# Performance work log

Measured on AMD Instinct MI355X. Metric: run time of the kernel, lower is better.

Reference implementation:

```python
import jax, jax.numpy as jnp
import numpy as np

B, IN, H = 8192, 1024, 1024

def _ln(x, g, b, eps=1e-5):
    mu = jnp.mean(x, axis=-1, keepdims=True)
    var = jnp.mean(jnp.square(x - mu), axis=-1, keepdims=True)
    return (x - mu) * jax.lax.rsqrt(var + eps) * g + b

def setup_inputs() -> dict:
    key = jax.random.key(0)
    ks = jax.random.split(key, 8)
    s_h = 1.0 / np.sqrt(H)
    s_i = 1.0 / np.sqrt(IN)
    inp = {
        'x': jax.random.normal(ks[0], (B, IN), jnp.float32),
        'h': jax.random.normal(ks[1], (B, H), jnp.float32),
        'W_r': jax.random.uniform(ks[2], (H, H), jnp.float32, -s_h, s_h),
        'U_r': jax.random.uniform(ks[3], (H, IN), jnp.float32, -s_i, s_i),
        'W_u': jax.random.uniform(ks[4], (H, H), jnp.float32, -s_h, s_h),
        'U_u': jax.random.uniform(ks[5], (H, IN), jnp.float32, -s_i, s_i),
        'W_c': jax.random.uniform(ks[6], (H, H), jnp.float32, -s_h, s_h),
        'U_c': jax.random.uniform(ks[7], (H, IN), jnp.float32, -s_i, s_i),
        # LayerNorm params: rows = [r_hidden, r_input, u_hidden, u_input, c_hidden, c_input]
        'ln_gamma': 0.1 * jnp.ones((6, H), jnp.float32),
        'ln_beta': jnp.zeros((6, H), jnp.float32),
    }
    return inp

def reference(x, h, W_r, U_r, W_u, U_u, W_c, U_c, ln_gamma, ln_beta):
    g, b = ln_gamma, ln_beta
    # nn.Linear(bias=False): y = x @ W.T
    r = jax.nn.sigmoid(_ln(h @ W_r.T, g[0], b[0]) + _ln(x @ U_r.T, g[1], b[1]))
    u = jax.nn.sigmoid(_ln(h @ W_u.T, g[2], b[2]) + _ln(x @ U_u.T, g[3], b[3]))
    c = jnp.tanh(_ln((h * r) @ W_c.T, g[4], b[4]) + _ln(x @ U_c.T, g[5], b[5]))
    return (1.0 - u) * h + u * c
```

## Files before the change

### kernel.cpp

```cpp
#include <hip/hip_runtime.h>
#include <cstdint>
#include <cstddef>

typedef unsigned short u16;
typedef unsigned char u8;
typedef __attribute__((ext_vector_type(4))) float f32x4;
typedef __attribute__((ext_vector_type(4))) int i32x4;
typedef __attribute__((ext_vector_type(8))) int i32x8;

__device__ inline float bf2f(u16 u) { return __uint_as_float(((unsigned)u) << 16); }
__device__ inline unsigned f2bf(float f) {
  unsigned u = __float_as_uint(f);
  u += 0x7fffu + ((u >> 16) & 1u);
  return u >> 16;
}

__device__ inline unsigned f2fp8(float f) {
  unsigned s = (__float_as_uint(f) >> 31) << 7;
  float a = fabsf(f);
  if (a >= 0.015625f) {
    unsigned u = __float_as_uint(a);
    u += 0x7FFFFu + ((u >> 20) & 1u);
    unsigned e = (u >> 23) - 120u;
    unsigned m = (u >> 20) & 7u;
    return s | (e << 3) | m;
  }
  int m = (int)rintf(a * 512.0f);
  return s | (unsigned)m;
}

__device__ inline void async16(const void* g, void* l) {
  __builtin_amdgcn_global_load_lds(
      (const __attribute__((address_space(1))) void*)g,
      (__attribute__((address_space(3))) void*)l, 16, 0, 0);
}

__device__ inline i32x8 join8(i32x4 lo, i32x4 hi) {
  i32x8 r;
  r[0] = lo[0]; r[1] = lo[1]; r[2] = lo[2]; r[3] = lo[3];
  r[4] = hi[0]; r[5] = hi[1]; r[6] = hi[2]; r[7] = hi[3];
  return r;
}

__device__ inline void unpack8(uint4 q, float* o) {
  o[0] = bf2f((u16)(q.x & 0xffffu)); o[1] = bf2f((u16)(q.x >> 16));
  o[2] = bf2f((u16)(q.y & 0xffffu)); o[3] = bf2f((u16)(q.y >> 16));
  o[4] = bf2f((u16)(q.z & 0xffffu)); o[5] = bf2f((u16)(q.z >> 16));
  o[6] = bf2f((u16)(q.w & 0xffffu)); o[7] = bf2f((u16)(q.w >> 16));
}

__device__ inline float fast_sigmoid(float z) {
  return 1.0f / (1.0f + exp2f(-1.4426950408889634f * z));
}
__device__ inline float fast_tanh(float z) {
  return 1.0f - 2.0f / (1.0f + exp2f(2.8853900817779268f * z));
}

#define SB0() __builtin_amdgcn_sched_barrier(0)

struct ConvArgs3 {
  const float* x; const float* h;
  const float* w[6];
  u8* x8; u8* h8;
  u8* w8[6];
};

__global__ __launch_bounds__(256) void convert_all(ConvArgs3 a) {
  const int b = blockIdx.x;
  const int t = threadIdx.x;
  if (b < 16384) {
    const bool isx = b < 8192;
    const int off = isx ? b : b - 8192;
    const float* __restrict__ s = isx ? a.x : a.h;
    u8* __restrict__ d8 = isx ? a.x8 : a.h8;
    const int i = (off * 256 + t) * 4;
    float4 v = *(const float4*)(s + i);
    unsigned q = f2fp8(v.x) | (f2fp8(v.y) << 8) | (f2fp8(v.z) << 16) | (f2fp8(v.w) << 24);
    *(unsigned*)(d8 + i) = q;
  } else {
    const int tt = b - 16384;
    const int which = tt >> 10;
    const int off = tt & 1023;
    const float* __restrict__ s = a.w[which];
    u8* __restrict__ d8 = a.w8[which];
    const int i = (off * 256 + t) * 4;
    float4 v = *(const float4*)(s + i);
    unsigned q = f2fp8(v.x * 8192.f) | (f2fp8(v.y * 8192.f) << 8) |
                 (f2fp8(v.z * 8192.f) << 16) | (f2fp8(v.w * 8192.f) << 24);
    *(unsigned*)(d8 + i) = q;
  }
}

struct GemmF8 { const u8* A[4]; const u8* Bw[4]; u16* Y[4]; };

template <int NG>
__global__ __launch_bounds__(512, 2) void gemm_fp8(GemmF8 args) {
  const int p = blockIdx.x;
  const int wg = (p & 7) * (NG * 16) + (p >> 3);
  const int gate = wg >> 7;
  const int rem  = wg & 127;
  const int rblk = rem >> 2;
  const int cblk = rem & 3;

  const u8* __restrict__ A  = args.A[gate];
  const u8* __restrict__ Bw = args.Bw[gate];
  u16* __restrict__ Y = args.Y[gate];

  __shared__ __attribute__((aligned(16))) u8 sm[2][2][2][128 * 128];

  const int tid  = threadIdx.x;
  const int lane = tid & 63;
  const int w    = tid >> 6;
  const int wm   = w >> 2;
  const int wn   = w & 3;

  const int l8   = lane >> 3;
  const int sgrp = (lane & 7) ^ l8;
  const u8* aSrc = A  + ((size_t)(rblk * 256 + w * 8 + l8) << 10) + sgrp * 16;
  const u8* bSrc = Bw + ((size_t)(cblk * 256 + w * 8 + l8) << 10) + sgrp * 16;
  const int ldsW = w * 8 * 128;

  const int sw = lane & 7;
  const int g0 = (lane >> 4) * 2;
  const int o0 = ((g0 ^ sw) << 4);
  const int o1 = (((g0 + 1) ^ sw) << 4);
  const int frR = (lane & 15) * 128;

  f32x4 acc_lo[4][4] = {};
  f32x4 acc_hi[4][4] = {};

  auto stage = [&](const u8* src, int tt, int op, int half) {
    const int d = tt & 1;
    const u8* s = src + (size_t)half * 131072 + tt * 128;
    u8* l0 = &sm[d][op][half][ldsW];
    async16(s, l0);
    async16(s + 65536, l0 + 8192);
  };

  stage(bSrc, 0, 1, 0); stage(bSrc, 0, 1, 1);
  stage(aSrc, 0, 0, 0); stage(aSrc, 0, 0, 1);
  stage(bSrc, 1, 1, 0); stage(bSrc, 1, 1, 1);
  stage(aSrc, 1, 0, 0);
  asm volatile("s_waitcnt vmcnt(6)" ::: "memory");
  __builtin_amdgcn_s_barrier();

  i32x8 alo[4], bfg[4], ahi[4];
  {
    const u8* baseA = &sm[0][0][wm][0];
    const u8* baseB = &sm[0][1][wn >> 1][(wn & 1) * 8192];
#pragma unroll
    for (int m = 0; m < 4; ++m) {
      const int ra = frR + m * 2048;
      alo[m] = join8(*(const i32x4*)&baseA[ra + o0], *(const i32x4*)&baseA[ra + o1]);
    }
#pragma unroll
    for (int n = 0; n < 4; ++n) {
      const int rbb = frR + n * 2048;
      bfg[n] = join8(*(const i32x4*)&baseB[rbb + o0], *(const i32x4*)&baseB[rbb + o1]);
    }
  }
  SB0();

  for (int t = 0; t < 8; ++t) {
    const int d = t & 1;
    const u8* baseA  = &sm[d][0][wm][0];
    const u8* baseA2 = &sm[d ^ 1][0][wm][0];
    const u8* baseB2 = &sm[d ^ 1][1][wn >> 1][(wn & 1) * 8192];

    if (t + 1 < 8) stage(aSrc, t + 1, 0, 1);
    SB0();
    __builtin_amdgcn_s_barrier();
    asm volatile("s_waitcnt lgkmcnt(4)" ::: "memory");
    SB0();
    __builtin_amdgcn_s_setprio(1);
#pragma unroll
    for (int m = 0; m < 4; ++m)
#pragma unroll
      for (int n = 0; n < 2; ++n)
        acc_lo[m][n] = __builtin_amdgcn_mfma_scale_f32_16x16x128_f8f6f4(
            alo[m], bfg[n], acc_lo[m][n], 0, 0, 0, 127, 0, 114);
    __builtin_amdgcn_s_setprio(0);
    SB0();
    __builtin_amdgcn_s_barrier();

    if (t + 2 < 8) stage(bSrc, t + 2, 1, 0);
    SB0();
    __builtin_amdgcn_s_barrier();
    asm volatile("s_waitcnt lgkmcnt(0)" ::: "memory");
    SB0();
    __builtin_amdgcn_s_setprio(1);
#pragma unroll
    for (int m = 0; m < 4; ++m)
#pragma unroll
      for (int n = 2; n < 4; ++n)
        acc_lo[m][n] = __builtin_amdgcn_mfma_scale_f32_16x16x128_f8f6f4(
            alo[m], bfg[n], acc_lo[m][n], 0, 0, 0, 127, 0, 114);
    __builtin_amdgcn_s_setprio(0);
    SB0();
#pragma unroll
    for (int m = 0; m < 4; ++m) {
      const int ra = frR + m * 2048 + 8192;
      ahi[m] = join8(*(const i32x4*)&baseA[ra + o0], *(const i32x4*)&baseA[ra + o1]);
    }
    SB0();
    __builtin_amdgcn_s_barrier();

    if (t + 2 < 8) stage(bSrc, t + 2, 1, 1);
    SB0();
    __builtin_amdgcn_s_barrier();
    asm volatile("s_waitcnt lgkmcnt(0)" ::: "memory");
    SB0();
    __builtin_amdgcn_s_setprio(1);
#pragma unroll
    for (int m = 0; m < 4; ++m)
#pragma unroll
      for (int n = 0; n < 2; ++n)
        acc_hi[m][n] = __builtin_amdgcn_mfma_scale_f32_16x16x128_f8f6f4(
            ahi[m], bfg[n], acc_hi[m][n], 0, 0, 0, 127, 0, 114);
    __builtin_amdgcn_s_setprio(0);
    SB0();
    __builtin_amdgcn_s_barrier();

    if (t + 2 < 8) stage(aSrc, t + 2, 0, 0);
    SB0();
    __builtin_amdgcn_s_barrier();
    __builtin_amdgcn_s_setprio(1);
#pragma unroll
    for (int m = 0; m < 4; ++m)
#pragma unroll
      for (int n = 2; n < 4; ++n)
        acc_hi[m][n] = __builtin_amdgcn_mfma_scale_f32_16x16x128_f8f6f4(
            ahi[m], bfg[n], acc_hi[m][n], 0, 0, 0, 127, 0, 114);
    __builtin_amdgcn_s_setprio(0);
    SB0();
    if (t < 6) asm volatile("s_waitcnt vmcnt(6)" ::: "memory");
    else       asm volatile("s_waitcnt vmcnt(0)" ::: "memory");
    SB0();
    if (t + 1 < 8) {
#pragma unroll
      for (int m = 0; m < 4; ++m) {
        const int ra = frR + m * 2048;
        alo[m] = join8(*(const i32x4*)&baseA2[ra + o0], *(const i32x4*)&baseA2[ra + o1]);
      }
#pragma unroll
      for (int n = 0; n < 4; ++n) {
        const int rbb = frR + n * 2048;
        bfg[n] = join8(*(const i32x4*)&baseB2[rbb + o0], *(const i32x4*)&baseB2[rbb + o1]);
      }
    }
    SB0();
    __builtin_amdgcn_s_barrier();
  }

  const int rBase = rblk * 256 + wm * 128 + (lane >> 4) * 4;
  const int cBase = cblk * 256 + wn * 64 + (lane & 15);
#pragma unroll
  for (int m = 0; m < 4; ++m) {
#pragma unroll
    for (int i = 0; i < 4; ++i) {
      const size_t r0 = (size_t)(rBase + m * 16 + i) * 1024 + cBase;
#pragma unroll
      for (int n = 0; n < 4; ++n) {
        Y[r0 + n * 16]             = (u16)f2bf(acc_lo[m][n][i]);
        Y[r0 + 64 * 1024 + n * 16] = (u16)f2bf(acc_hi[m][n][i]);
      }
    }
  }
}

__global__ __launch_bounds__(256) void rgate_kernel(
    const u16* __restrict__ Yrh, const u16* __restrict__ Yrx,
    const float* __restrict__ h, const float* __restrict__ gamma,
    const float* __restrict__ beta, u8* __restrict__ hr8) {
  const int row  = blockIdx.x * 4 + (threadIdx.x >> 6);
  const int lane = threadIdx.x & 63;
  const size_t rb = (size_t)row * 1024;

  uint4 qa[2], qb[2];
  float4 hf[4];
#pragma unroll
  for (int c = 0; c < 2; c++) {
    const int cb = c * 512 + lane * 8;
    qa[c] = *(const uint4*)(Yrh + rb + cb);
    qb[c] = *(const uint4*)(Yrx + rb + cb);
    hf[c * 2]     = *(const float4*)(h + rb + cb);
    hf[c * 2 + 1] = *(const float4*)(h + rb + cb + 4);
  }

  float s0 = 0.f, s0q = 0.f, s1 = 0.f, s1q = 0.f;
  float tmp[8];
#pragma unroll
  for (int c = 0; c < 2; c++) {
    unpack8(qa[c], tmp);
#pragma unroll
    for (int j = 0; j < 8; j++) { s0 += tmp[j]; s0q += tmp[j] * tmp[j]; }
    unpack8(qb[c], tmp);
#pragma unroll
    for (int j = 0; j < 8; j++) { s1 += tmp[j]; s1q += tmp[j] * tmp[j]; }
  }
#pragma unroll
  for (int off = 1; off < 64; off <<= 1) {
    s0 += __shfl_xor(s0, off, 64);  s0q += __shfl_xor(s0q, off, 64);
    s1 += __shfl_xor(s1, off, 64);  s1q += __shfl_xor(s1q, off, 64);
  }

  const float inv = 1.0f / 1024.0f;
  const float mu0 = s0 * inv, rs0 = rsqrtf(s0q * inv - mu0 * mu0 + 1e-5f);
  const float mu1 = s1 * inv, rs1 = rsqrtf(s1q * inv - mu1 * mu1 + 1e-5f);

#pragma unroll
  for (int c = 0; c < 2; c++) {
    const int cb = c * 512 + lane * 8;
    float va[8], vb[8], o[8];
    unpack8(qa[c], va); unpack8(qb[c], vb);
    const float* hv = (const float*)&hf[c * 2];
#pragma unroll
    for (int j = 0; j < 8; j++) {
      const float ln0 = (va[j] - mu0) * rs0 * gamma[cb + j] + beta[cb + j];
      const float ln1 = (vb[j] - mu1) * rs1 * gamma[1024 + cb + j] + beta[1024 + cb + j];
      const float rg = fast_sigmoid(ln0 + ln1);
      o[j] = hv[j] * rg;
    }
    uint2 q;
    q.x = f2fp8(o[0]) | (f2fp8(o[1]) << 8) | (f2fp8(o[2]) << 16) | (f2fp8(o[3]) << 24);
    q.y = f2fp8(o[4]) | (f2fp8(o[5]) << 8) | (f2fp8(o[6]) << 16) | (f2fp8(o[7]) << 24);
    *(uint2*)(hr8 + rb + cb) = q;
  }
}

__global__ __launch_bounds__(256) void final_fuse(
    const u16* __restrict__ Yuh, const u16* __restrict__ Yux,
    const u16* __restrict__ Ych, const u16* __restrict__ Ycx,
    const float* __restrict__ h, const float* __restrict__ gamma,
    const float* __restrict__ beta, float* __restrict__ out) {
  const int row  = blockIdx.x * 4 + (threadIdx.x >> 6);
  const int lane = threadIdx.x & 63;
  const size_t rb = (size_t)row * 1024;

  uint4 q0[2], q1[2], q2[2], q3[2];
  float4 hf[4];
#pragma unroll
  for (int c = 0; c < 2; c++) {
    const int cb = c * 512 + lane * 8;
    q0[c] = *(const uint4*)(Yuh + rb + cb);
    q1[c] = *(const uint4*)(Yux + rb + cb);
    q2[c] = *(const uint4*)(Ych + rb + cb);
    q3[c] = *(const uint4*)(Ycx + rb + cb);
    hf[c * 2]     = *(const float4*)(h + rb + cb);
    hf[c * 2 + 1] = *(const float4*)(h + rb + cb + 4);
  }

  float s[8] = {0.f, 0.f, 0.f, 0.f, 0.f, 0.f, 0.f, 0.f};
  float tmp[8];
#pragma unroll
  for (int c = 0; c < 2; c++) {
    unpack8(q0[c], tmp);
#pragma unroll
    for (int j = 0; j < 8; j++) { s[0] += tmp[j]; s[1] += tmp[j] * tmp[j]; }
    unpack8(q1[c], tmp);
#pragma unroll
    for (int j = 0; j < 8; j++) { s[2] += tmp[j]; s[3] += tmp[j] * tmp[j]; }
    unpack8(q2[c], tmp);
#pragma unroll
    for (int j = 0; j < 8; j++) { s[4] += tmp[j]; s[5] += tmp[j] * tmp[j]; }
    unpack8(q3[c], tmp);
#pragma unroll
    for (int j = 0; j < 8; j++) { s[6] += tmp[j]; s[7] += tmp[j] * tmp[j]; }
  }
#pragma unroll
  for (int off = 1; off < 64; off <<= 1) {
#pragma unroll
    for (int q = 0; q < 8; q++) s[q] += __shfl_xor(s[q], off, 64);
  }

  const float inv = 1.0f / 1024.0f;
  const float mu0 = s[0] * inv, rs0 = rsqrtf(s[1] * inv - mu0 * mu0 + 1e-5f);
  const float mu1 = s[2] * inv, rs1 = rsqrtf(s[3] * inv - mu1 * mu1 + 1e-5f);
  const float mu2 = s[4] * inv, rs2 = rsqrtf(s[5] * inv - mu2 * mu2 + 1e-5f);
  const float mu3 = s[6] * inv, rs3 = rsqrtf(s[7] * inv - mu3 * mu3 + 1e-5f);

#pragma unroll
  for (int c = 0; c < 2; c++) {
    const int cb = c * 512 + lane * 8;
    float v0[8], v1[8], v2[8], v3[8];
    unpack8(q0[c], v0); unpack8(q1[c], v1); unpack8(q2[c], v2); unpack8(q3[c], v3);
    const float* hv = (const float*)&hf[c * 2];
    float o[8];
#pragma unroll
    for (int j = 0; j < 8; j++) {
      const int cc = cb + j;
      const float ln2 = (v0[j] - mu0) * rs0 * gamma[2 * 1024 + cc] + beta[2 * 1024 + cc];
      const float ln3 = (v1[j] - mu1) * rs1 * gamma[3 * 1024 + cc] + beta[3 * 1024 + cc];
      const float ln4 = (v2[j] - mu2) * rs2 * gamma[4 * 1024 + cc] + beta[4 * 1024 + cc];
      const float ln5 = (v3[j] - mu3) * rs3 * gamma[5 * 1024 + cc] + beta[5 * 1024 + cc];
      const float u  = fast_sigmoid(ln2 + ln3);
      const float cg = fast_tanh(ln4 + ln5);
      o[j] = (1.0f - u) * hv[j] + u * cg;
    }
    *(float4*)(out + rb + cb)     = *(float4*)&o[0];
    *(float4*)(out + rb + cb + 4) = *(float4*)&o[4];
  }
}

extern "C" void kernel_launch(void* const* d_in, const int* in_sizes, int n_in,
                              void* d_out, int out_size, void* d_ws, size_t ws_size,
                              hipStream_t stream) {
  const float* x  = (const float*)d_in[0];
  const float* h  = (const float*)d_in[1];
  const float* W_r = (const float*)d_in[2];
  const float* U_r = (const float*)d_in[3];
  const float* W_u = (const float*)d_in[4];
  const float* U_u = (const float*)d_in[5];
  const float* W_c = (const float*)d_in[6];
  const float* U_c = (const float*)d_in[7];
  const float* gamma = (const float*)d_in[8];
  const float* beta  = (const float*)d_in[9];
  float* out = (float*)d_out;

  char* ws = (char*)d_ws;
  const size_t MB = 1024 * 1024;

  u8* x8  = (u8*)(ws);
  u8* h8  = (u8*)(ws + 8 * MB);
  u8* hr8 = (u8*)(ws + 16 * MB);
  u8* w8[6];
  for (int i = 0; i < 6; i++) w8[i] = (u8*)(ws + 24 * MB + i * MB);
  u16* Y0 = (u16*)(ws + 32 * MB);
  u16* Y1 = (u16*)(ws + 48 * MB);
  u16* Y2 = (u16*)(ws + 64 * MB);
  u16* Y3 = (u16*)(ws + 80 * MB);
  u16* Y5 = (u16*)(ws + 96 * MB);

  ConvArgs3 ca = {};
  ca.x = x; ca.h = h;
  ca.w[0] = W_r; ca.w[1] = U_r; ca.w[2] = W_u; ca.w[3] = U_u; ca.w[4] = W_c; ca.w[5] = U_c;
  ca.x8 = x8; ca.h8 = h8;
  for (int i = 0; i < 6; i++) ca.w8[i] = w8[i];
  convert_all<<<22528, 256, 0, stream>>>(ca);

  GemmF8 gA = {};
  gA.A[0] = h8; gA.Bw[0] = w8[0]; gA.Y[0] = Y0;
  gA.A[1] = x8; gA.Bw[1] = w8[1]; gA.Y[1] = Y1;
  gA.A[2] = x8; gA.Bw[2] = w8[3]; gA.Y[2] = Y3;
  gA.A[3] = x8; gA.Bw[3] = w8[5]; gA.Y[3] = Y5;
  gemm_fp8<4><<<512, 512, 0, stream>>>(gA);

  rgate_kernel<<<2048, 256, 0, stream>>>(Y0, Y1, h, gamma, beta, hr8);

  GemmF8 gB = {};
  gB.A[0] = h8;  gB.Bw[0] = w8[2]; gB.Y[0] = Y2;
  gB.A[1] = hr8; gB.Bw[1] = w8[4]; gB.Y[1] = Y0;
  gemm_fp8<2><<<256, 512, 0, stream>>>(gB);

  final_fuse<<<2048, 256, 0, stream>>>(Y2, Y3, Y0, Y5, h, gamma, beta, out);
}
```

Before: 241.3 us.

## Shrink FP8 GEMM tiles to 128x128 with 4 waves and simpler double buffering

```diff
diff --git a/kernel.cpp b/kernel.cpp
--- a/kernel.cpp
+++ b/kernel.cpp
@@ -94,176 +94,103 @@
 struct GemmF8 { const u8* A[4]; const u8* Bw[4]; u16* Y[4]; };
 
 template <int NG>
-__global__ __launch_bounds__(512, 2) void gemm_fp8(GemmF8 args) {
+__global__ __launch_bounds__(256, 2) void gemm_f8s(GemmF8 args) {
   const int p = blockIdx.x;
-  const int wg = (p & 7) * (NG * 16) + (p >> 3);
-  const int gate = wg >> 7;
-  const int rem  = wg & 127;
-  const int rblk = rem >> 2;
-  const int cblk = rem & 3;
+  const int wg = (p & 7) * (NG * 64) + (p >> 3);
+  const int gate = wg >> 9;
+  const int rem  = wg & 511;
+  const int rblk = rem >> 3;
+  const int cblk = rem & 7;
 
   const u8* __restrict__ A  = args.A[gate];
   const u8* __restrict__ Bw = args.Bw[gate];
   u16* __restrict__ Y = args.Y[gate];
 
-  __shared__ __attribute__((aligned(16))) u8 sm[2][2][2][128 * 128];
+  __shared__ __attribute__((aligned(16))) u8 smA[2][128 * 128];
+  __shared__ __attribute__((aligned(16))) u8 smB[2][128 * 128];
 
   const int tid  = threadIdx.x;
   const int lane = tid & 63;
   const int w    = tid >> 6;
-  const int wm   = w >> 2;
-  const int wn   = w & 3;
+  const int wm   = w >> 1;
+  const int wn   = w & 1;
 
   const int l8   = lane >> 3;
   const int sgrp = (lane & 7) ^ l8;
-  const u8* aSrc = A  + ((size_t)(rblk * 256 + w * 8 + l8) << 10) + sgrp * 16;
-  const u8* bSrc = Bw + ((size_t)(cblk * 256 + w * 8 + l8) << 10) + sgrp * 16;
-  const int ldsW = w * 8 * 128;
+  const u8* aSrc = A  + ((size_t)(rblk * 128 + w * 32 + l8) << 10) + sgrp * 16;
+  const u8* bSrc = Bw + ((size_t)(cblk * 128 + w * 32 + l8) << 10) + sgrp * 16;
 
   const int sw = lane & 7;
   const int g0 = (lane >> 4) * 2;
   const int o0 = ((g0 ^ sw) << 4);
   const int o1 = (((g0 + 1) ^ sw) << 4);
-  const int frR = (lane & 15) * 128;
-
-  f32x4 acc_lo[4][4] = {};
-  f32x4 acc_hi[4][4] = {};
-
-  auto stage = [&](const u8* src, int tt, int op, int half) {
-    const int d = tt & 1;
-    const u8* s = src + (size_t)half * 131072 + tt * 128;
-    u8* l0 = &sm[d][op][half][ldsW];
-    async16(s, l0);
-    async16(s + 65536, l0 + 8192);
+  const int frA = (wm * 64 + (lane & 15)) * 128;
+  const int frB = (wn * 64 + (lane & 15)) * 128;
+
+  f32x4 acc[4][4] = {};
+
+  auto stage = [&](int tt) {
+    const int cur = tt & 1;
+    const size_t ko = (size_t)tt * 128;
+#pragma unroll
+    for (int i = 0; i < 4; ++i) {
+      async16(aSrc + (size_t)i * 8192 + ko, &smA[cur][(w * 32 + i * 8) * 128]);
+      async16(bSrc + (size_t)i * 8192 + ko, &smB[cur][(w * 32 + i * 8) * 128]);
+    }
   };
 
-  stage(bSrc, 0, 1, 0); stage(bSrc, 0, 1, 1);
-  stage(aSrc, 0, 0, 0); stage(aSrc, 0, 0, 1);
-  stage(bSrc, 1, 1, 0); stage(bSrc, 1, 1, 1);
-  stage(aSrc, 1, 0, 0);
-  asm volatile("s_waitcnt vmcnt(6)" ::: "memory");
+  stage(0);
+  stage(1);
+  asm volatile("s_waitcnt vmcnt(8)" ::: "memory");
   __builtin_amdgcn_s_barrier();
 
-  i32x8 alo[4], bfg[4], ahi[4];
-  {
-    const u8* baseA = &sm[0][0][wm][0];
-    const u8* baseB = &sm[0][1][wn >> 1][(wn & 1) * 8192];
+  for (int t = 0; t < 8; ++t) {
+    const int cur = t & 1;
+    const u8* bA = &smA[cur][0];
+    const u8* bB = &smB[cur][0];
+
+    i32x8 af[4], bf[4];
 #pragma unroll
     for (int m = 0; m < 4; ++m) {
-      const int ra = frR + m * 2048;
-      alo[m] = join8(*(const i32x4*)&baseA[ra + o0], *(const i32x4*)&baseA[ra + o1]);
+      const int ra = frA + m * 2048;
+      af[m] = join8(*(const i32x4*)&bA[ra + o0], *(const i32x4*)&bA[ra + o1]);
     }
 #pragma unroll
     for (int n = 0; n < 4; ++n) {
-      const int rbb = frR + n * 2048;
-      bfg[n] = join8(*(const i32x4*)&baseB[rbb + o0], *(const i32x4*)&baseB[rbb + o1]);
-    }
-  }
-  SB0();
-
-  for (int t = 0; t < 8; ++t) {
-    const int d = t & 1;
-    const u8* baseA  = &sm[d][0][wm][0];
-    const u8* baseA2 = &sm[d ^ 1][0][wm][0];
-    const u8* baseB2 = &sm[d ^ 1][1][wn >> 1][(wn & 1) * 8192];
-
-    if (t + 1 < 8) stage(aSrc, t + 1, 0, 1);
+      const int rb = frB + n * 2048;
+      bf[n] = join8(*(const i32x4*)&bB[rb + o0], *(const i32x4*)&bB[rb + o1]);
+    }
+    asm volatile("s_waitcnt lgkmcnt(0)" ::: "memory");
     SB0();
     __builtin_amdgcn_s_barrier();
-    asm volatile("s_waitcnt lgkmcnt(4)" ::: "memory");
+
+    if (t + 2 < 8) stage(t + 2);
     SB0();
     __builtin_amdgcn_s_setprio(1);
 #pragma unroll
     for (int m = 0; m < 4; ++m)
 #pragma unroll
-      for (int n = 0; n < 2; ++n)
-        acc_lo[m][n] = __builtin_amdgcn_mfma_scale_f32_16x16x128_f8f6f4(
-            alo[m], bfg[n], acc_lo[m][n], 0, 0, 0, 127, 0, 114);
+      for (int n = 0; n < 4; ++n)
+        acc[m][n] = __builtin_amdgcn_mfma_scale_f32_16x16x128_f8f6f4(
+            af[m], bf[n], acc[m][n], 0, 0, 0, 127, 0, 114);
     __builtin_amdgcn_s_setprio(0);
     SB0();
-    __builtin_amdgcn_s_barrier();
-
-    if (t + 2 < 8) stage(bSrc, t + 2, 1, 0);
+    if (t < 6)      asm volatile("s_waitcnt vmcnt(8)" ::: "memory");
+    else if (t == 6) asm volatile("s_waitcnt vmcnt(0)" ::: "memory");
     SB0();
     __builtin_amdgcn_s_barrier();
-    asm volatile("s_waitcnt lgkmcnt(0)" ::: "memory");
-    SB0();
-    __builtin_amdgcn_s_setprio(1);
-#pragma unroll
-    for (int m = 0; m < 4; ++m)
-#pragma unroll
-      for (int n = 2; n < 4; ++n)
-        acc_lo[m][n] = __builtin_amdgcn_mfma_scale_f32_16x16x128_f8f6f4(
-            alo[m], bfg[n], acc_lo[m][n], 0, 0, 0, 127, 0, 114);
-    __builtin_amdgcn_s_setprio(0);
-    SB0();
-#pragma unroll
-    for (int m = 0; m < 4; ++m) {
-      const int ra = frR + m * 2048 + 8192;
-      ahi[m] = join8(*(const i32x4*)&baseA[ra + o0], *(const i32x4*)&baseA[ra + o1]);
-    }
-    SB0();
-    __builtin_amdgcn_s_barrier();
-
-    if (t + 2 < 8) stage(bSrc, t + 2, 1, 1);
-    SB0();
-    __builtin_amdgcn_s_barrier();
-    asm volatile("s_waitcnt lgkmcnt(0)" ::: "memory");
-    SB0();
-    __builtin_amdgcn_s_setprio(1);
-#pragma unroll
-    for (int m = 0; m < 4; ++m)
-#pragma unroll
-      for (int n = 0; n < 2; ++n)
-        acc_hi[m][n] = __builtin_amdgcn_mfma_scale_f32_16x16x128_f8f6f4(
-            ahi[m], bfg[n], acc_hi[m][n], 0, 0, 0, 127, 0, 114);
-    __builtin_amdgcn_s_setprio(0);
-    SB0();
-    __builtin_amdgcn_s_barrier();
-
-    if (t + 2 < 8) stage(aSrc, t + 2, 0, 0);
-    SB0();
-    __builtin_amdgcn_s_barrier();
-    __builtin_amdgcn_s_setprio(1);
-#pragma unroll
-    for (int m = 0; m < 4; ++m)
-#pragma unroll
-      for (int n = 2; n < 4; ++n)
-        acc_hi[m][n] = __builtin_amdgcn_mfma_scale_f32_16x16x128_f8f6f4(
-            ahi[m], bfg[n], acc_hi[m][n], 0, 0, 0, 127, 0, 114);
-    __builtin_amdgcn_s_setprio(0);
-    SB0();
-    if (t < 6) asm volatile("s_waitcnt vmcnt(6)" ::: "memory");
-    else       asm volatile("s_waitcnt vmcnt(0)" ::: "memory");
-    SB0();
-    if (t + 1 < 8) {
-#pragma unroll
-      for (int m = 0; m < 4; ++m) {
-        const int ra = frR + m * 2048;
-        alo[m] = join8(*(const i32x4*)&baseA2[ra + o0], *(const i32x4*)&baseA2[ra + o1]);
-      }
-#pragma unroll
-      for (int n = 0; n < 4; ++n) {
-        const int rbb = frR + n * 2048;
-        bfg[n] = join8(*(const i32x4*)&baseB2[rbb + o0], *(const i32x4*)&baseB2[rbb + o1]);
-      }
-    }
-    SB0();
-    __builtin_amdgcn_s_barrier();
-  }
-
-  const int rBase = rblk * 256 + wm * 128 + (lane >> 4) * 4;
-  const int cBase = cblk * 256 + wn * 64 + (lane & 15);
+  }
+
+  const int rBase = rblk * 128 + wm * 64 + (lane >> 4) * 4;
+  const int cBase = cblk * 128 + wn * 64 + (lane & 15);
 #pragma unroll
   for (int m = 0; m < 4; ++m) {
 #pragma unroll
     for (int i = 0; i < 4; ++i) {
       const size_t r0 = (size_t)(rBase + m * 16 + i) * 1024 + cBase;
 #pragma unroll
-      for (int n = 0; n < 4; ++n) {
-        Y[r0 + n * 16]             = (u16)f2bf(acc_lo[m][n][i]);
-        Y[r0 + 64 * 1024 + n * 16] = (u16)f2bf(acc_hi[m][n][i]);
-      }
+      for (int n = 0; n < 4; ++n)
+        Y[r0 + n * 16] = (u16)f2bf(acc[m][n][i]);
     }
   }
 }
@@ -443,14 +370,14 @@
   gA.A[1] = x8; gA.Bw[1] = w8[1]; gA.Y[1] = Y1;
   gA.A[2] = x8; gA.Bw[2] = w8[3]; gA.Y[2] = Y3;
   gA.A[3] = x8; gA.Bw[3] = w8[5]; gA.Y[3] = Y5;
-  gemm_fp8<4><<<512, 512, 0, stream>>>(gA);
+  gemm_f8s<4><<<2048, 256, 0, stream>>>(gA);
 
   rgate_kernel<<<2048, 256, 0, stream>>>(Y0, Y1, h, gamma, beta, hr8);
 
   GemmF8 gB = {};
   gB.A[0] = h8;  gB.Bw[0] = w8[2]; gB.Y[0] = Y2;
   gB.A[1] = hr8; gB.Bw[1] = w8[4]; gB.Y[1] = Y0;
-  gemm_fp8<2><<<256, 512, 0, stream>>>(gB);
+  gemm_f8s<2><<<1024, 256, 0, stream>>>(gB);
 
   final_fuse<<<2048, 256, 0, stream>>>(Y2, Y3, Y0, Y5, h, gamma, beta, out);
 }
```

New measurement: 246.2 us. +2.0%, slower.
